# Performance work log

Hardware: AMD Instinct MI355X
Metric: run time of the kernel (lower is better)

Reference implementation:

```python
import jax, jax.numpy as jnp
import numpy as np

Q_DIM = 1024
K_DIM = 1024
EMBED_DIM = 1024
NUM_HEADS = 16
HEAD_DIM = EMBED_DIM // NUM_HEADS
SCALE = HEAD_DIM ** (-0.5)
CLAMP = 50000.0
MASK_NEG = -9e15


def _xavier(key, out_f, in_f):
    limit = float(np.sqrt(6.0 / (in_f + out_f)))
    return jax.random.uniform(key, (out_f, in_f), jnp.float32, -limit, limit)


def setup_inputs() -> dict:
    key = jax.random.key(0)
    ks = jax.random.split(key, 8)
    B, Tq, Tk = 4, 2048, 2048
    return {
        "q": jax.random.normal(ks[0], (B, Tq, Q_DIM), jnp.float32),
        "k": jax.random.normal(ks[1], (B, Tk, K_DIM), jnp.float32),
        "v": jax.random.normal(ks[2], (B, Tk, K_DIM), jnp.float32),
        "attention_mask": jax.random.randint(ks[3], (B, Tk), 0, 2, jnp.int32),
        "Wq": _xavier(ks[4], EMBED_DIM, Q_DIM),
        "bq": jnp.zeros((EMBED_DIM,), jnp.float32),
        "Wk": _xavier(ks[5], EMBED_DIM, K_DIM),
        "bk": jnp.zeros((EMBED_DIM,), jnp.float32),
        "Wv": _xavier(ks[6], EMBED_DIM, K_DIM),
        "bv": jnp.zeros((EMBED_DIM,), jnp.float32),
        "Wo": _xavier(ks[7], K_DIM, EMBED_DIM),
        "bo": jnp.zeros((K_DIM,), jnp.float32),
    }


def _split_heads(x, B, T):
    # [B, T, E] -> [B, H, T, D]
    return x.reshape(B, T, NUM_HEADS, HEAD_DIM).transpose(0, 2, 1, 3)


def reference(q, k, v, attention_mask, Wq, bq, Wk, bk, Wv, bv, Wo, bo):
    B, Tq, _ = q.shape
    Tk = k.shape[1]
    # projections (nn.Linear: x @ W.T + b)
    qs = _split_heads((q @ Wq.T + bq) * SCALE, B, Tq)   # [B,H,Tq,D]
    ks_ = _split_heads(k @ Wk.T + bk, B, Tk)            # [B,H,Tk,D]
    vs = _split_heads(v @ Wv.T + bv, B, Tk)             # [B,H,Tk,D]
    # scores with clamp
    scores = jnp.einsum("bhqd,bhkd->bhqk", qs, ks_)
    scores = jnp.clip(scores, -CLAMP, CLAMP)
    # additive mask: masked_fill(mask==0, -9e15) then add (nonzero entries add their value)
    m = attention_mask.astype(scores.dtype)
    add_mask = jnp.where(attention_mask == 0, MASK_NEG, m)  # [B,Tk]
    scores = scores + add_mask[:, None, None, :]
    probs = jax.nn.softmax(scores, axis=-1)
    # dropout inactive in eval mode
    attn = jnp.einsum("bhqk,bhkd->bhqd", probs, vs)
    attn = attn.transpose(0, 2, 1, 3).reshape(B, Tq, EMBED_DIM)
    return attn @ Wo.T + bo
```

## Files before the change

### kernel.cpp

```cpp
#include <hip/hip_runtime.h>
#include <hip/hip_bf16.h>

typedef __bf16 bf16x8 __attribute__((ext_vector_type(8)));
typedef float  f32x4  __attribute__((ext_vector_type(4)));
typedef unsigned short ushort;
typedef ushort ushort4v __attribute__((ext_vector_type(4)));

#if __has_builtin(__builtin_amdgcn_exp2f)
#define EXP2(x) __builtin_amdgcn_exp2f(x)
#else
#define EXP2(x) exp2f(x)
#endif

__device__ __forceinline__ ushort f2bf(float f) {
  union { float f; unsigned u; } v; v.f = f;
  unsigned r = v.u + 0x7FFFu + ((v.u >> 16) & 1u);
  return (ushort)(r >> 16);
}

typedef __attribute__((address_space(1))) const unsigned int as1_uint;
typedef __attribute__((address_space(3))) unsigned int as3_uint;
__device__ __forceinline__ void gll16(const void* g, void* l) {
  __builtin_amdgcn_global_load_lds((as1_uint*)g, (as3_uint*)l, 16, 0, 0);
}

__global__ void prep_all(const float* __restrict__ Wq, const float* __restrict__ Wk,
                         const float* __restrict__ Wv, const float* __restrict__ Wo,
                         const float* __restrict__ q, const float* __restrict__ k,
                         const float* __restrict__ v, const int* __restrict__ mask,
                         ushort4v* __restrict__ wqb, ushort4v* __restrict__ wkb,
                         ushort4v* __restrict__ wvb, ushort4v* __restrict__ wob,
                         ushort4v* __restrict__ qb, ushort4v* __restrict__ kb,
                         ushort4v* __restrict__ vb, float* __restrict__ madd) {
  int y = blockIdx.y;
  if (y == 4) {
    int i = blockIdx.x * blockDim.x + threadIdx.x;
    if (i < 8192) {
      int mv = mask[i];
      madd[i] = (mv == 0) ? -9e15f * 1.44269504f : (float)mv * 1.44269504f;
    }
    return;
  }
  const float* s; ushort4v* d; int n4;
  if (y < 4) {
    s = (y == 0) ? Wq : (y == 1) ? Wk : (y == 2) ? Wv : Wo;
    d = (y == 0) ? wqb : (y == 1) ? wkb : (y == 2) ? wvb : wob;
    n4 = 1024 * 1024 / 4;
  } else {
    s = (y == 5) ? q : (y == 6) ? k : v;
    d = (y == 5) ? qb : (y == 6) ? kb : vb;
    n4 = 8192 * 1024 / 4;
  }
  const float4* s4p = (const float4*)s;
  for (int i = blockIdx.x * blockDim.x + threadIdx.x; i < n4; i += gridDim.x * blockDim.x) {
    float4 vv = s4p[i]; ushort4v o;
    o[0] = f2bf(vv.x); o[1] = f2bf(vv.y); o[2] = f2bf(vv.z); o[3] = f2bf(vv.w);
    d[i] = o;
  }
}

__device__ __forceinline__ void gemm_core(
    const ushort* __restrict__ A, const ushort* __restrict__ W,
    const float* __restrict__ bias, void* __restrict__ outp,
    float scale, int mode, ushort* smem)
{
  const int tid = threadIdx.x, lane = tid & 63, wid = tid >> 6;
  const int r0 = blockIdx.x * 128, c0 = blockIdx.y * 128;
  const int wr = (wid >> 1) * 64, wc = (wid & 1) * 64;
  const int K = 1024;
  ushort* sA = smem;
  ushort* sB = smem + 8192;

  f32x4 acc[4][4] = {};

  for (int kt = 0; kt < 16; ++kt) {
    const int k0 = kt * 64;
#pragma unroll
    for (int i = 0; i < 4; ++i) {
      int s = (wid * 4 + i) * 64 + lane;
      int row = s >> 3, sl = s & 7, gsl = sl ^ (row & 7);
      gll16(&A[(size_t)(r0 + row) * K + k0 + gsl * 8], &sA[(wid * 4 + i) * 512]);
      gll16(&W[(size_t)(c0 + row) * K + k0 + gsl * 8], &sB[(wid * 4 + i) * 512]);
    }
    __syncthreads();
#pragma unroll
    for (int kk = 0; kk < 2; ++kk) {
      bf16x8 af[4], bf[4];
#pragma unroll
      for (int mf = 0; mf < 4; ++mf) {
        int row = wr + mf * 16 + (lane & 15);
        int slot = (kk * 4 + (lane >> 4)) ^ (row & 7);
        af[mf] = *(const bf16x8*)&sA[row * 64 + slot * 8];
      }
#pragma unroll
      for (int nf = 0; nf < 4; ++nf) {
        int row = wc + nf * 16 + (lane & 15);
        int slot = (kk * 4 + (lane >> 4)) ^ (row & 7);
        bf[nf] = *(const bf16x8*)&sB[row * 64 + slot * 8];
      }
#pragma unroll
      for (int mf = 0; mf < 4; ++mf)
#pragma unroll
        for (int nf = 0; nf < 4; ++nf)
          acc[mf][nf] = __builtin_amdgcn_mfma_f32_16x16x32_bf16(af[mf], bf[nf], acc[mf][nf], 0, 0, 0);
    }
    __syncthreads();
  }

  if (mode == 2) {
    ushort* sT = smem;
#pragma unroll
    for (int nf = 0; nf < 4; ++nf) {
      int col = wc + nf * 16 + (lane & 15);
      float bv = bias[c0 + col];
#pragma unroll
      for (int mf = 0; mf < 4; ++mf)
#pragma unroll
        for (int r = 0; r < 4; ++r) {
          int row = wr + mf * 16 + ((lane >> 4) * 4) + r;
          sT[col * 128 + (row ^ ((col & 7) << 3))] = f2bf(acc[mf][nf][r] + bv);
        }
    }
    __syncthreads();
    int bidx = r0 >> 11, tb = r0 & 2047;
#pragma unroll
    for (int it = 0; it < 8; ++it) {
      int colr = it * 16 + wid * 4 + (lane >> 4);
      int t0 = (lane & 15) * 8;
      int4 v = *(const int4*)&sT[colr * 128 + (t0 ^ ((colr & 7) << 3))];
      int colg = c0 + colr;
      int hh = colg >> 6, d = colg & 63;
      *(int4*)&((ushort*)outp)[((size_t)(bidx * 16 + hh) * 64 + d) * 2048 + tb + t0] = v;
    }
    return;
  }

#pragma unroll
  for (int nf = 0; nf < 4; ++nf) {
    int col = c0 + wc + nf * 16 + (lane & 15);
    float bv = bias[col];
#pragma unroll
    for (int mf = 0; mf < 4; ++mf) {
#pragma unroll
      for (int r = 0; r < 4; ++r) {
        int row = r0 + wr + mf * 16 + ((lane >> 4) * 4) + r;
        float v = (acc[mf][nf][r] + bv) * scale;
        if (mode == 0) {
          int b = row >> 11, t = row & 2047;
          int h = col >> 6, d = col & 63;
          ((ushort*)outp)[(((size_t)(b * 16 + h) * 2048 + t) << 6) + d] = f2bf(v);
        } else {
          ((float*)outp)[(size_t)row * 1024 + col] = v;
        }
      }
    }
  }
}

__global__ __launch_bounds__(256) void gemm3(
    const ushort* __restrict__ qb, const ushort* __restrict__ kb, const ushort* __restrict__ vb,
    const ushort* __restrict__ wq, const ushort* __restrict__ wk, const ushort* __restrict__ wv,
    const float* __restrict__ bq, const float* __restrict__ bk, const float* __restrict__ bv,
    ushort* __restrict__ Qs, ushort* __restrict__ Ks, ushort* __restrict__ Vts)
{
  __shared__ __align__(16) ushort smem[16384];
  int z = blockIdx.z;
  const ushort *A, *W; const float* bias; ushort* out; float scale; int mode;
  if (z == 0)      { A = qb; W = wq; bias = bq; out = Qs;  scale = 0.125f * 1.44269504f; mode = 0; }
  else if (z == 1) { A = kb; W = wk; bias = bk; out = Ks;  scale = 1.0f;   mode = 0; }
  else             { A = vb; W = wv; bias = bv; out = Vts; scale = 1.0f;   mode = 2; }
  gemm_core(A, W, bias, out, scale, mode, smem);
}

__global__ __launch_bounds__(256) void gemmF(
    const ushort* __restrict__ Oat, const ushort* __restrict__ wo,
    const float* __restrict__ bo, float* __restrict__ out)
{
  __shared__ __align__(16) ushort smem[16384];
  gemm_core(Oat, wo, bo, out, 1.0f, 1, smem);
}

__global__ __launch_bounds__(256) void attn(
    const ushort* __restrict__ Q, const ushort* __restrict__ Km,
    const ushort* __restrict__ Vt, const float* __restrict__ madd,
    ushort* __restrict__ O)
{
  __shared__ __align__(16) ushort sK[2][64 * 64];
  __shared__ __align__(16) ushort sV[2][64 * 64];

  const int tid = threadIdx.x, lane = tid & 63, wid = tid >> 6;
  const int bid = blockIdx.x;
  const int x = bid & 7, g = bid >> 3;
  const int pair = x * 8 + (g >> 5), qt = g & 31;
  const int b = pair >> 4, h = pair & 15;

  const size_t hb = (size_t)pair * (2048 * 64);
  const ushort* Qh = Q + hb + (size_t)qt * (64 * 64);
  const ushort* Kh = Km + hb;
  const ushort* Vh = Vt + hb;
  const float* mb = madd + b * 2048;

  const int m = lane & 15, qg = lane >> 4;

#define STAGE(BSEL, T) do {                                                     \
    const int n0g_ = (T) * 64;                                                  \
    _Pragma("unroll")                                                           \
    for (int i_ = 0; i_ < 2; ++i_) {                                            \
      int ch_ = wid * 2 + i_;                                                   \
      int s_ = ch_ * 64 + lane;                                                 \
      int row_ = s_ >> 3, sl_ = s_ & 7, gsl_ = sl_ ^ (row_ & 7);                \
      gll16(&Kh[(size_t)(n0g_ + row_) * 64 + gsl_ * 8], &sK[BSEL][ch_ * 512]);  \
      gll16(&Vh[(size_t)row_ * 2048 + n0g_ + gsl_ * 8], &sV[BSEL][ch_ * 512]);  \
    }                                                                           \
  } while (0)

  bf16x8 qf[2];
#pragma unroll
  for (int kk = 0; kk < 2; ++kk)
    qf[kk] = *(const bf16x8*)&Qh[(size_t)(wid * 16 + m) * 64 + kk * 32 + qg * 8];

  f32x4 mreg[4];
#pragma unroll
  for (int af = 0; af < 4; ++af)
    mreg[af] = *(const f32x4*)&mb[af * 16 + qg * 4];

  union { unsigned u[4]; bf16x8 v; } onesu;
  onesu.u[0] = onesu.u[1] = onesu.u[2] = onesu.u[3] = 0x3F803F80u;
  const bf16x8 ones = onesu.v;

  STAGE(0, 0);
  __syncthreads();

  float runm = -3.0e38f;
  f32x4 o[4] = {};
  f32x4 osum = {};

#define TILE_BODY(BK, BV, KT) do {                                              \
    f32x4 s4_[4];                                                               \
    _Pragma("unroll")                                                           \
    for (int af = 0; af < 4; ++af) s4_[af] = mreg[af];                          \
    if ((KT) < 31) {                                                            \
      const float* ms_ = mb + ((KT) + 1) * 64 + qg * 4;                         \
      _Pragma("unroll")                                                         \
      for (int af = 0; af < 4; ++af) mreg[af] = *(const f32x4*)&ms_[af * 16];   \
    }                                                                           \
    __builtin_amdgcn_s_setprio(1);                                              \
    _Pragma("unroll")                                                           \
    for (int af = 0; af < 4; ++af) {                                            \
      _Pragma("unroll")                                                         \
      for (int kk = 0; kk < 2; ++kk) {                                          \
        int krow_ = af * 16 + m;                                                \
        int slot_ = (kk * 4 + qg) ^ (krow_ & 7);                                \
        bf16x8 kf_ = *(const bf16x8*)&(BK)[krow_ * 64 + slot_ * 8];             \
        s4_[af] = __builtin_amdgcn_mfma_f32_16x16x32_bf16(kf_, qf[kk], s4_[af], 0, 0, 0); \
      }                                                                         \
    }                                                                           \
    __builtin_amdgcn_s_setprio(0);                                              \
    float tmax_ = fmaxf(fmaxf(s4_[0][0], s4_[0][1]), fmaxf(s4_[0][2], s4_[0][3])); \
    _Pragma("unroll")                                                           \
    for (int af = 1; af < 4; ++af)                                              \
      tmax_ = fmaxf(tmax_, fmaxf(fmaxf(s4_[af][0], s4_[af][1]),                 \
                                 fmaxf(s4_[af][2], s4_[af][3])));               \
    tmax_ = fmaxf(tmax_, __shfl_xor(tmax_, 16, 64));                            \
    tmax_ = fmaxf(tmax_, __shfl_xor(tmax_, 32, 64));                            \
    if (!__all(tmax_ <= runm + 11.5416f)) {                                     \
      float newm_ = fmaxf(runm, tmax_);                                         \
      float corr_ = EXP2(runm - newm_);                                         \
      osum[0] *= corr_;                                                         \
      _Pragma("unroll")                                                         \
      for (int af = 0; af < 4; ++af) o[af] *= corr_;                            \
      runm = newm_;                                                             \
    }                                                                           \
    unsigned w_[4][2];                                                          \
    _Pragma("unroll")                                                           \
    for (int af = 0; af < 4; ++af) {                                            \
      _Pragma("unroll")                                                         \
      for (int r = 0; r < 4; ++r) s4_[af][r] = EXP2(s4_[af][r] - runm);         \
      asm("v_cvt_pk_bf16_f32 %0, %1, %2"                                        \
          : "=v"(w_[af][0]) : "v"(s4_[af][0]), "v"(s4_[af][1]));                \
      asm("v_cvt_pk_bf16_f32 %0, %1, %2"                                        \
          : "=v"(w_[af][1]) : "v"(s4_[af][2]), "v"(s4_[af][3]));                \
    }                                                                           \
    __builtin_amdgcn_s_setprio(1);                                              \
    _Pragma("unroll")                                                           \
    for (int kk = 0; kk < 2; ++kk) {                                            \
      unsigned a0_ = w_[2 * kk][0], a1_ = w_[2 * kk][1];                        \
      unsigned b0_ = w_[2 * kk + 1][0], b1_ = w_[2 * kk + 1][1];                \
      asm("v_permlane32_swap_b32 %0, %1" : "+v"(a0_), "+v"(b0_));               \
      asm("v_permlane16_swap_b32 %0, %1" : "+v"(a0_), "+v"(b0_));               \
      asm("v_permlane32_swap_b32 %0, %1" : "+v"(a1_), "+v"(b1_));               \
      asm("v_permlane16_swap_b32 %0, %1" : "+v"(a1_), "+v"(b1_));               \
      union { unsigned u[4]; bf16x8 v; } pu_;                                   \
      pu_.u[0] = a0_; pu_.u[1] = a1_; pu_.u[2] = b0_; pu_.u[3] = b1_;           \
      bf16x8 pf_ = pu_.v;                                                       \
      osum = __builtin_amdgcn_mfma_f32_16x16x32_bf16(ones, pf_, osum, 0, 0, 0); \
      _Pragma("unroll")                                                         \
      for (int af = 0; af < 4; ++af) {                                          \
        int drow_ = af * 16 + m;                                                \
        int slot_ = (kk * 4 + qg) ^ (drow_ & 7);                                \
        bf16x8 vf_ = *(const bf16x8*)&(BV)[drow_ * 64 + slot_ * 8];             \
        o[af] = __builtin_amdgcn_mfma_f32_16x16x32_bf16(vf_, pf_, o[af], 0, 0, 0); \
      }                                                                         \
    }                                                                           \
    __builtin_amdgcn_s_setprio(0);                                              \
  } while (0)

  for (int it = 0; it < 16; ++it) {
    const int kt0 = 2 * it;
    STAGE(1, kt0 + 1);
    TILE_BODY(sK[0], sV[0], kt0);
    __syncthreads();

    const int kt1 = kt0 + 1;
    if (kt1 < 31) STAGE(0, kt1 + 1);
    TILE_BODY(sK[1], sV[1], kt1);
    __syncthreads();
  }
#undef TILE_BODY
#undef STAGE

  float inv = 1.0f / osum[0];
  int tq = qt * 64 + wid * 16 + m;
  size_t obase = (((size_t)(b * 2048 + tq)) * 16 + h) * 64;
#pragma unroll
  for (int af = 0; af < 4; ++af) {
    ushort4v pk;
#pragma unroll
    for (int r = 0; r < 4; ++r) pk[r] = f2bf(o[af][r] * inv);
    *(ushort4v*)&O[obase + af * 16 + qg * 4] = pk;
  }
}

extern "C" void kernel_launch(void* const* d_in, const int* in_sizes, int n_in,
                              void* d_out, int out_size, void* d_ws, size_t ws_size,
                              hipStream_t stream) {
  const float* q  = (const float*)d_in[0];
  const float* k  = (const float*)d_in[1];
  const float* v  = (const float*)d_in[2];
  const int* mask = (const int*)d_in[3];
  const float* Wq = (const float*)d_in[4];
  const float* bq = (const float*)d_in[5];
  const float* Wk = (const float*)d_in[6];
  const float* bk = (const float*)d_in[7];
  const float* Wv = (const float*)d_in[8];
  const float* bv = (const float*)d_in[9];
  const float* Wo = (const float*)d_in[10];
  const float* bo = (const float*)d_in[11];
  float* out = (float*)d_out;

  const size_t NEED = (size_t)104 << 20;
  if (ws_size < NEED) return;

  char* ws = (char*)d_ws;
  ushort* WQb = (ushort*)(ws + ((size_t)0 << 20));
  ushort* WKb = (ushort*)(ws + ((size_t)2 << 20));
  ushort* WVb = (ushort*)(ws + ((size_t)4 << 20));
  ushort* WOb = (ushort*)(ws + ((size_t)6 << 20));
  ushort* qb  = (ushort*)(ws + ((size_t)8 << 20));
  ushort* kb  = (ushort*)(ws + ((size_t)24 << 20));
  ushort* vb  = (ushort*)(ws + ((size_t)40 << 20));
  ushort* Qs  = (ushort*)(ws + ((size_t)56 << 20));
  ushort* Ks  = (ushort*)(ws + ((size_t)72 << 20));
  ushort* Vts = (ushort*)(ws + ((size_t)88 << 20));
  ushort* Oat = qb;
  float* madd = (float*)d_out;

  prep_all<<<dim3(1024, 8), dim3(256), 0, stream>>>(Wq, Wk, Wv, Wo, q, k, v, mask,
      (ushort4v*)WQb, (ushort4v*)WKb, (ushort4v*)WVb, (ushort4v*)WOb,
      (ushort4v*)qb, (ushort4v*)kb, (ushort4v*)vb, madd);

  gemm3<<<dim3(64, 8, 3), dim3(256), 0, stream>>>(qb, kb, vb, WQb, WKb, WVb,
      bq, bk, bv, Qs, Ks, Vts);

  attn<<<dim3(2048), dim3(256), 0, stream>>>(Qs, Ks, Vts, madd, Oat);

  gemmF<<<dim3(64, 8), dim3(256), 0, stream>>>(Oat, WOb, bo, out);
}
```

Before: 242.3 us.

## Load K/V fragments directly from global memory, dropping LDS staging and barriers

The attention kernel no longer stages K and V tiles into double-buffered shared memory with global_load_lds and __syncthreads. Each wave now reads its MFMA operand fragments straight from global memory through advancing pointers, relying on L2/L1 caching for reuse across the four waves of a block. The mask prefetch is split into two ping-pong register sets. This removes LDS traffic and block-wide synchronization, but each wave now issues its own global loads, which are redundant across waves. It also drops the explicit prefetch of the next tile, so more memory latency may be exposed.

```diff
diff --git a/kernel.cpp b/kernel.cpp
--- a/kernel.cpp
+++ b/kernel.cpp
@@ -185,9 +185,6 @@
     const ushort* __restrict__ Vt, const float* __restrict__ madd,
     ushort* __restrict__ O)
 {
-  __shared__ __align__(16) ushort sK[2][64 * 64];
-  __shared__ __align__(16) ushort sV[2][64 * 64];
-
   const int tid = threadIdx.x, lane = tid & 63, wid = tid >> 6;
   const int bid = blockIdx.x;
   const int x = bid & 7, g = bid >> 3;
@@ -196,64 +193,47 @@
 
   const size_t hb = (size_t)pair * (2048 * 64);
   const ushort* Qh = Q + hb + (size_t)qt * (64 * 64);
-  const ushort* Kh = Km + hb;
-  const ushort* Vh = Vt + hb;
   const float* mb = madd + b * 2048;
 
   const int m = lane & 15, qg = lane >> 4;
 
-#define STAGE(BSEL, T) do {                                                     \
-    const int n0g_ = (T) * 64;                                                  \
-    _Pragma("unroll")                                                           \
-    for (int i_ = 0; i_ < 2; ++i_) {                                            \
-      int ch_ = wid * 2 + i_;                                                   \
-      int s_ = ch_ * 64 + lane;                                                 \
-      int row_ = s_ >> 3, sl_ = s_ & 7, gsl_ = sl_ ^ (row_ & 7);                \
-      gll16(&Kh[(size_t)(n0g_ + row_) * 64 + gsl_ * 8], &sK[BSEL][ch_ * 512]);  \
-      gll16(&Vh[(size_t)row_ * 2048 + n0g_ + gsl_ * 8], &sV[BSEL][ch_ * 512]);  \
-    }                                                                           \
-  } while (0)
+  const ushort* Kp = Km + hb + (size_t)m * 64 + qg * 8;
+  const ushort* Vp = Vt + hb + (size_t)m * 2048 + qg * 8;
 
   bf16x8 qf[2];
 #pragma unroll
   for (int kk = 0; kk < 2; ++kk)
     qf[kk] = *(const bf16x8*)&Qh[(size_t)(wid * 16 + m) * 64 + kk * 32 + qg * 8];
 
-  f32x4 mreg[4];
+  f32x4 mA[4], mB[4];
 #pragma unroll
   for (int af = 0; af < 4; ++af)
-    mreg[af] = *(const f32x4*)&mb[af * 16 + qg * 4];
+    mA[af] = *(const f32x4*)&mb[af * 16 + qg * 4];
 
   union { unsigned u[4]; bf16x8 v; } onesu;
   onesu.u[0] = onesu.u[1] = onesu.u[2] = onesu.u[3] = 0x3F803F80u;
   const bf16x8 ones = onesu.v;
 
-  STAGE(0, 0);
-  __syncthreads();
-
   float runm = -3.0e38f;
   f32x4 o[4] = {};
   f32x4 osum = {};
 
-#define TILE_BODY(BK, BV, KT) do {                                              \
+#define TILE_BODY(MC, MN, KT) do {                                              \
     f32x4 s4_[4];                                                               \
     _Pragma("unroll")                                                           \
-    for (int af = 0; af < 4; ++af) s4_[af] = mreg[af];                          \
+    for (int af = 0; af < 4; ++af) s4_[af] = MC[af];                            \
     if ((KT) < 31) {                                                            \
       const float* ms_ = mb + ((KT) + 1) * 64 + qg * 4;                         \
       _Pragma("unroll")                                                         \
-      for (int af = 0; af < 4; ++af) mreg[af] = *(const f32x4*)&ms_[af * 16];   \
+      for (int af = 0; af < 4; ++af) MN[af] = *(const f32x4*)&ms_[af * 16];     \
     }                                                                           \
     __builtin_amdgcn_s_setprio(1);                                              \
     _Pragma("unroll")                                                           \
     for (int af = 0; af < 4; ++af) {                                            \
-      _Pragma("unroll")                                                         \
-      for (int kk = 0; kk < 2; ++kk) {                                          \
-        int krow_ = af * 16 + m;                                                \
-        int slot_ = (kk * 4 + qg) ^ (krow_ & 7);                                \
-        bf16x8 kf_ = *(const bf16x8*)&(BK)[krow_ * 64 + slot_ * 8];             \
-        s4_[af] = __builtin_amdgcn_mfma_f32_16x16x32_bf16(kf_, qf[kk], s4_[af], 0, 0, 0); \
-      }                                                                         \
+      bf16x8 kf0_ = *(const bf16x8*)&Kp[af * 1024];                             \
+      bf16x8 kf1_ = *(const bf16x8*)&Kp[af * 1024 + 32];                        \
+      s4_[af] = __builtin_amdgcn_mfma_f32_16x16x32_bf16(kf0_, qf[0], s4_[af], 0, 0, 0); \
+      s4_[af] = __builtin_amdgcn_mfma_f32_16x16x32_bf16(kf1_, qf[1], s4_[af], 0, 0, 0); \
     }                                                                           \
     __builtin_amdgcn_s_setprio(0);                                              \
     float tmax_ = fmaxf(fmaxf(s4_[0][0], s4_[0][1]), fmaxf(s4_[0][2], s4_[0][3])); \
@@ -296,28 +276,21 @@
       osum = __builtin_amdgcn_mfma_f32_16x16x32_bf16(ones, pf_, osum, 0, 0, 0); \
       _Pragma("unroll")                                                         \
       for (int af = 0; af < 4; ++af) {                                          \
-        int drow_ = af * 16 + m;                                                \
-        int slot_ = (kk * 4 + qg) ^ (drow_ & 7);                                \
-        bf16x8 vf_ = *(const bf16x8*)&(BV)[drow_ * 64 + slot_ * 8];             \
+        bf16x8 vf_ = *(const bf16x8*)&Vp[af * 32768 + kk * 32];                 \
         o[af] = __builtin_amdgcn_mfma_f32_16x16x32_bf16(vf_, pf_, o[af], 0, 0, 0); \
       }                                                                         \
     }                                                                           \
     __builtin_amdgcn_s_setprio(0);                                              \
+    Kp += 4096;                                                                 \
+    Vp += 64;                                                                   \
   } while (0)
 
   for (int it = 0; it < 16; ++it) {
     const int kt0 = 2 * it;
-    STAGE(1, kt0 + 1);
-    TILE_BODY(sK[0], sV[0], kt0);
-    __syncthreads();
-
-    const int kt1 = kt0 + 1;
-    if (kt1 < 31) STAGE(0, kt1 + 1);
-    TILE_BODY(sK[1], sV[1], kt1);
-    __syncthreads();
+    TILE_BODY(mA, mB, kt0);
+    TILE_BODY(mB, mA, kt0 + 1);
   }
 #undef TILE_BODY
-#undef STAGE
 
   float inv = 1.0f / osum[0];
   int tq = qt * 64 + wid * 16 + m;
```

Measured after the change: 655.0 us. 170% more time.
